# Kernel optimization log

Measured on AMD Instinct MI355X. Metric: run time of the kernel, lower is better.

## Reference

```python
import itertools
import jax, jax.numpy as jnp
import numpy as np

# static block configuration
B, C, H, W, DIM, HEADS = 2, 4, 60, 120, 512, 8
WS = (2, 6, 12)          # window size (Wc, Wh, Ww)
SS = (1, 3, 6)           # shift size
N = WS[0] * WS[1] * WS[2]            # 144 tokens per window
C1, H1, W1 = C // WS[0], H // WS[1], W // WS[2]
NW = C1 * H1 * W1                    # windows per sample
DH = DIM // HEADS
EPS = 1e-6


def _attn_bias():
    """Static shifted-window attention bias (nW, N, N): 0 within group, -inf across.
    Mirrors compute_3d_shifted_window_mask (warped=True, longitude wrap merge)."""
    img = np.zeros((C, H, W), np.int32)
    c_sl = ((0, C - WS[0]), (C - WS[0], C - SS[0]), (C - SS[0], C))
    h_sl = ((0, H - WS[1]), (H - WS[1], H - SS[1]), (H - SS[1], H))
    w_sl = ((0, W - WS[2]), (W - WS[2], W - SS[2]), (W - SS[2], W))
    cnt = 0
    for (cs, ce), (hs, he), (ws_, we) in itertools.product(c_sl, h_sl, w_sl):
        img[cs:ce, hs:he, ws_:we] = cnt
        cnt += 1
    # warped (periodic longitude) group merges
    for i in range(3):
        for a, b in ((1, 2), (4, 5), (7, 8)):
            img[img == a + 9 * i] = b + 9 * i
    m = img.reshape(C1, WS[0], H1, WS[1], W1, WS[2])
    m = m.transpose(0, 2, 4, 1, 3, 5).reshape(NW, N)
    diff = m[:, None, :] - m[:, :, None]
    return jnp.asarray(np.where(diff != 0, -np.inf, 0.0).astype(np.float32))


_BIAS = _attn_bias()[None, :, None, :, :]  # (1, nW, 1, N, N)


def _ln(x, s, b):
    mu = x.mean(-1, keepdims=True)
    var = x.var(-1, keepdims=True)
    return (x - mu) / jnp.sqrt(var + EPS) * s + b


def setup_inputs() -> dict:
    key = jax.random.key(0)
    ks = jax.random.split(key, 6)
    s = 0.02
    return {
        "x": jax.random.normal(ks[0], (B, C * H * W, DIM), jnp.float32),
        "qkv_w": jax.random.normal(ks[1], (DIM, 3 * DIM), jnp.float32) * s,
        "qkv_b": jnp.zeros((3 * DIM,), jnp.float32),
        "proj_w": jax.random.normal(ks[2], (DIM, DIM), jnp.float32) * s,
        "proj_b": jnp.zeros((DIM,), jnp.float32),
        "norm1_scale": jnp.ones((DIM,), jnp.float32),
        "norm1_bias": jnp.zeros((DIM,), jnp.float32),
        "norm2_scale": jnp.ones((DIM,), jnp.float32),
        "norm2_bias": jnp.zeros((DIM,), jnp.float32),
        "mlp_w1": jax.random.normal(ks[3], (DIM, 4 * DIM), jnp.float32) * s,
        "mlp_b1": jnp.zeros((4 * DIM,), jnp.float32),
        "mlp_w2": jax.random.normal(ks[4], (4 * DIM, DIM), jnp.float32) * s,
        "mlp_b2": jnp.zeros((DIM,), jnp.float32),
    }


def reference(x, qkv_w, qkv_b, proj_w, proj_b, norm1_scale, norm1_bias,
              norm2_scale, norm2_bias, mlp_w1, mlp_b1, mlp_w2, mlp_b2):
    shortcut = x                                   # (B, L, D)
    h = _ln(x, norm1_scale, norm1_bias).reshape(B, C, H, W, DIM)
    # cyclic shift
    h = jnp.roll(h, (-SS[0], -SS[1], -SS[2]), axis=(1, 2, 3))
    # window partition: (B,C,H,W,D) -> (B*nW, N, D)
    h = h.reshape(B, C1, WS[0], H1, WS[1], W1, WS[2], DIM)
    h = h.transpose(0, 1, 3, 5, 2, 4, 6, 7).reshape(B * NW, N, DIM)
    # windowed multi-head self-attention
    qkv = h @ qkv_w + qkv_b                        # (B*nW, N, 3*D)
    qkv = qkv.reshape(B, NW, N, 3, HEADS, DH)
    q = qkv[..., 0, :, :].transpose(0, 1, 3, 2, 4)  # (B, nW, H, N, Dh)
    k = qkv[..., 1, :, :].transpose(0, 1, 3, 2, 4)
    v = qkv[..., 2, :, :].transpose(0, 1, 3, 2, 4)
    scale = 1.0 / float(np.sqrt(DH))
    attn = jnp.einsum("bwhnd,bwhmd->bwhnm", q, k) * scale + _BIAS
    attn = jax.nn.softmax(attn, axis=-1)
    o = jnp.einsum("bwhnm,bwhmd->bwhnd", attn, v)
    o = o.transpose(0, 1, 3, 2, 4).reshape(B * NW, N, DIM)
    o = o @ proj_w + proj_b
    # window reverse: (B*nW, N, D) -> (B,C,H,W,D)
    o = o.reshape(B, C1, H1, W1, WS[0], WS[1], WS[2], DIM)
    o = o.transpose(0, 1, 4, 2, 5, 3, 6, 7).reshape(B, C, H, W, DIM)
    # reverse cyclic shift
    o = jnp.roll(o, SS, axis=(1, 2, 3))
    x = shortcut + o.reshape(B, C * H * W, DIM)    # drop_path is identity
    # MLP block
    h2 = _ln(x, norm2_scale, norm2_bias)
    h2 = jax.nn.gelu(h2 @ mlp_w1 + mlp_b1) @ mlp_w2 + mlp_b2
    return x + h2
```

## Files before the change

### kernel.cpp

```cpp
#include <hip/hip_runtime.h>

typedef __attribute__((ext_vector_type(4))) int i32x4;
typedef __attribute__((ext_vector_type(8))) short bf16x8;
typedef __attribute__((ext_vector_type(4))) float f32x4;
typedef __attribute__((ext_vector_type(8))) unsigned short u16x8;
typedef __attribute__((ext_vector_type(8))) char c8x8;

#define BAR() __builtin_amdgcn_s_barrier()
#define VMC(n) asm volatile("s_waitcnt vmcnt(" #n ")" ::: "memory")
#define SB0() __builtin_amdgcn_sched_barrier(0)
#define WAITL() do { asm volatile("s_waitcnt lgkmcnt(0)"); SB0(); } while (0)
#define DSRI(dst, base, imm) \
  asm volatile("ds_read_b128 %0, %1 offset:%2" : "=&v"(dst) : "v"(base), "i"(imm))

__device__ inline unsigned short f2bf(float f) {
  unsigned int u = __float_as_uint(f);
  u += 0x7fffu + ((u >> 16) & 1u);
  return (unsigned short)(u >> 16);
}

__device__ inline char q8(float v, float s) {
  float q = rintf(v * s);
  q = fminf(fmaxf(q, -127.0f), 127.0f);
  return (char)(int)q;
}

__device__ inline void gload_lds16(const void* g, void* l) {
  __builtin_amdgcn_global_load_lds(
      (const __attribute__((address_space(1))) void*)g,
      (__attribute__((address_space(3))) void*)l, 16, 0, 0);
}

__global__ void zero4(unsigned* p) {
  if (threadIdx.x < 4) p[threadIdx.x] = 0;
}

__global__ void wabsmax(const float* __restrict__ a, const float* __restrict__ b,
                        const float* __restrict__ c, const float* __restrict__ d,
                        unsigned* __restrict__ sc) {
  int blk = blockIdx.x;
  const float* W;
  int seg;
  size_t base;
  if (blk < 768) { W = a; seg = 0; base = (size_t)blk * 1024; }
  else if (blk < 1024) { W = b; seg = 1; base = (size_t)(blk - 768) * 1024; }
  else if (blk < 2048) { W = c; seg = 2; base = (size_t)(blk - 1024) * 1024; }
  else { W = d; seg = 3; base = (size_t)(blk - 2048) * 1024; }
  float m = 0.0f;
  #pragma unroll
  for (int i = 0; i < 4; ++i)
    m = fmaxf(m, fabsf(W[base + threadIdx.x * 4 + i]));
  #pragma unroll
  for (int o = 32; o; o >>= 1) m = fmaxf(m, __shfl_xor(m, o));
  if ((threadIdx.x & 63) == 0) atomicMax(&sc[seg], __float_as_uint(m));
}

__global__ void wtrans_all(const float* __restrict__ qkv_w,
                           const float* __restrict__ proj_w,
                           const float* __restrict__ w1,
                           const float* __restrict__ w2,
                           char* __restrict__ WqT, char* __restrict__ WpT,
                           char* __restrict__ W1T, char* __restrict__ W2T,
                           const unsigned* __restrict__ sc) {
  int idx = blockIdx.x * 256 + threadIdx.x;
  const float* W;
  char* Wt;
  int K, N, seg;
  if (idx < 786432) {
    W = qkv_w; Wt = WqT; K = 512; N = 1536; seg = 0;
  } else if (idx < 1048576) {
    idx -= 786432; W = proj_w; Wt = WpT; K = 512; N = 512; seg = 1;
  } else if (idx < 2097152) {
    idx -= 1048576; W = w1; Wt = W1T; K = 512; N = 2048; seg = 2;
  } else {
    idx -= 2097152; W = w2; Wt = W2T; K = 2048; N = 512; seg = 3;
  }
  float wabs = __uint_as_float(sc[seg]);
  int k = idx / N, n = idx - k * N;
  Wt[(size_t)n * K + k] = q8(W[idx], 127.0f / wabs);
}

template <int MODE>
__global__ void ln_k(const float* __restrict__ x, const float* __restrict__ sc,
                     const float* __restrict__ bi, char* __restrict__ o) {
  int t = blockIdx.x * 4 + (threadIdx.x >> 6);
  int l = threadIdx.x & 63;
  size_t src;
  if (MODE == 0) {
    int b = t / 28800, r = t - b * 28800;
    int win = r / 144, tok = r - win * 144;
    int c1 = win / 100, rem = win - c1 * 100;
    int h1 = rem / 10, w1 = rem - h1 * 10;
    int tc = tok / 72, tr = tok - tc * 72;
    int th = tr / 12, tw = tr - th * 12;
    int cs = c1 * 2 + tc, hs = h1 * 6 + th, wsp = w1 * 12 + tw;
    int co = (cs + 1) & 3;
    int ho = hs + 3; if (ho >= 60) ho -= 60;
    int wo = wsp + 6; if (wo >= 120) wo -= 120;
    src = ((size_t)b * 28800 + (co * 60 + ho) * 120 + wo) * 512;
  } else {
    src = (size_t)t * 512;
  }
  const float4* xr = (const float4*)(x + src);
  float4 v0 = xr[l * 2], v1 = xr[l * 2 + 1];
  float s = v0.x + v0.y + v0.z + v0.w + v1.x + v1.y + v1.z + v1.w;
  float s2 = v0.x * v0.x + v0.y * v0.y + v0.z * v0.z + v0.w * v0.w +
             v1.x * v1.x + v1.y * v1.y + v1.z * v1.z + v1.w * v1.w;
  #pragma unroll
  for (int o2 = 32; o2; o2 >>= 1) {
    s += __shfl_xor(s, o2);
    s2 += __shfl_xor(s2, o2);
  }
  float mean = s * (1.0f / 512.0f);
  float var = s2 * (1.0f / 512.0f) - mean * mean;
  float inv = rsqrtf(var + 1e-6f);
  const float4* scp = (const float4*)sc;
  const float4* bip = (const float4*)bi;
  float4 sa = scp[l * 2], sb = scp[l * 2 + 1];
  float4 ba = bip[l * 2], bb = bip[l * 2 + 1];
  const float QS = 127.0f / 6.0f;
  c8x8 ov;
  ov[0] = q8((v0.x - mean) * inv * sa.x + ba.x, QS);
  ov[1] = q8((v0.y - mean) * inv * sa.y + ba.y, QS);
  ov[2] = q8((v0.z - mean) * inv * sa.z + ba.z, QS);
  ov[3] = q8((v0.w - mean) * inv * sa.w + ba.w, QS);
  ov[4] = q8((v1.x - mean) * inv * sb.x + bb.x, QS);
  ov[5] = q8((v1.y - mean) * inv * sb.y + bb.y, QS);
  ov[6] = q8((v1.z - mean) * inv * sb.z + bb.z, QS);
  ov[7] = q8((v1.w - mean) * inv * sb.w + bb.w, QS);
  *(c8x8*)&o[(size_t)t * 512 + l * 8] = ov;
}

template <int EPI>
__launch_bounds__(256, 2)
__global__ void gemmQ(const char* __restrict__ A, const char* __restrict__ Bt,
                      const float* __restrict__ bias, void* __restrict__ outp,
                      const float* __restrict__ res,
                      const unsigned* __restrict__ scu, int widx, float ascale,
                      int M, int N, int K) {
  __shared__ __attribute__((aligned(16))) char lds3[3][24576];
  const int tid = threadIdx.x;
  const int w = tid >> 6, l = tid & 63;
  const int lane15 = l & 15;
  const int ntile = N >> 8;
  const int nwg = gridDim.x;
  const int q = nwg >> 3, r = nwg & 7;
  const int xcd = blockIdx.x & 7, idx8 = blockIdx.x >> 3;
  const int wgid = (xcd < r ? xcd * (q + 1) : r * (q + 1) + (xcd - r) * q) + idx8;
  const int bm = wgid / ntile, bn = wgid - bm * ntile;
  const int KT = K >> 6;

  const int rA0 = w * 16 + (l >> 2);
  const int rA1 = (4 + w) * 16 + (l >> 2);
  const int colx0 = ((l & 3) << 4) ^ (((rA0 >> 1) & 3) << 4);
  const int offA0 = rA0 * K + colx0;
  const int offA1 = rA1 * K + colx0;
  int offB[4];
  #pragma unroll
  for (int j = 0; j < 4; ++j) {
    int rb = (j * 4 + w) * 16 + (l >> 2);
    offB[j] = rb * K + (((l & 3) << 4) ^ (((rb >> 1) & 3) << 4));
  }

  unsigned lds0 = (unsigned)(unsigned long long)
      (__attribute__((address_space(3))) void*)(void*)&lds3[0][0];
  const unsigned comA =
      (unsigned)(lane15 * 64 + (((l >> 4) << 4) ^ (((lane15 >> 1) & 3) << 4)));
  unsigned bA0 = lds0 + comA;
  unsigned bA1 = bA0 + 24576u, bA2 = bA0 + 49152u;
  const unsigned bOffB = 8192u + ((unsigned)w << 12);
  unsigned bB0 = bA0 + bOffB, bB1 = bA1 + bOffB, bB2 = bA2 + bOffB;

  char* p0 = &lds3[0][0];
  char* p1 = &lds3[1][0];
  char* p2 = &lds3[2][0];

  const char* gA = A + (size_t)bm * 128 * K;
  const char* gB = Bt + (size_t)bn * 256 * K;

  i32x4 acc[8][4] = {};
  i32x4 afL[4], afH[4], bfr[4];

  auto STAGE = [&](char* pS, const char* ga, const char* gb) {
    gload_lds16(ga + offA0, pS + w * 1024);
    gload_lds16(ga + offA1, pS + 4096 + w * 1024);
    #pragma unroll
    for (int j = 0; j < 4; ++j)
      gload_lds16(gb + offB[j], pS + 8192 + (j * 4 + w) * 1024);
  };

  STAGE(p0, gA, gB); gA += 64; gB += 64;
  STAGE(p1, gA, gB); gA += 64; gB += 64;
  VMC(6);
  BAR();

  for (int t = 0; t < KT; ++t) {
    if (t < KT - 2) {
      STAGE(p2, gA, gB);
      gA += 64; gB += 64;
    }
    DSRI(afL[0], bA0, 0);    DSRI(afL[1], bA0, 1024);
    DSRI(afL[2], bA0, 2048); DSRI(afL[3], bA0, 3072);
    DSRI(bfr[0], bB0, 0);    DSRI(bfr[1], bB0, 1024);
    DSRI(bfr[2], bB0, 2048); DSRI(bfr[3], bB0, 3072);
    WAITL();
    DSRI(afH[0], bA0, 4096); DSRI(afH[1], bA0, 5120);
    DSRI(afH[2], bA0, 6144); DSRI(afH[3], bA0, 7168);
    SB0();
    __builtin_amdgcn_s_setprio(1);
    #pragma unroll
    for (int mf = 0; mf < 4; ++mf)
      #pragma unroll
      for (int nf = 0; nf < 4; ++nf)
        acc[mf][nf] = __builtin_amdgcn_mfma_i32_16x16x64_i8(
            afL[mf], bfr[nf], acc[mf][nf], 0, 0, 0);
    __builtin_amdgcn_s_setprio(0);
    WAITL();
    __builtin_amdgcn_s_setprio(1);
    #pragma unroll
    for (int mf = 0; mf < 4; ++mf)
      #pragma unroll
      for (int nf = 0; nf < 4; ++nf)
        acc[4 + mf][nf] = __builtin_amdgcn_mfma_i32_16x16x64_i8(
            afH[mf], bfr[nf], acc[4 + mf][nf], 0, 0, 0);
    __builtin_amdgcn_s_setprio(0);
    if (t < KT - 2) { VMC(6); } else if (t == KT - 2) { VMC(0); }
    if (t < KT - 1) BAR();
    unsigned ta = bA0; bA0 = bA1; bA1 = bA2; bA2 = ta;
    unsigned tb = bB0; bB0 = bB1; bB1 = bB2; bB2 = tb;
    char* tp = p0; p0 = p1; p1 = p2; p2 = tp;
  }

  const float wabs = __uint_as_float(scu[widx]);
  const float fs = ascale * wabs * (1.0f / 127.0f);
  float* outf = (float*)outp;
  unsigned short* outh = (unsigned short*)outp;
  char* outc = (char*)outp;
  #pragma unroll
  for (int mi = 0; mi < 8; ++mi) {
    #pragma unroll
    for (int j = 0; j < 4; ++j) {
      int grow = bm * 128 + mi * 16 + ((l >> 4) << 2) + j;
      int win = 0, tok = 0;
      size_t rowbase = 0;
      if constexpr (EPI == 0) {
        win = grow / 144;
        tok = grow - win * 144;
      } else if constexpr (EPI == 1) {
        win = grow / 144;
        tok = grow - win * 144;
        int b = win / 200, wl = win - b * 200;
        int c1 = wl / 100, rem = wl - c1 * 100;
        int h1 = rem / 10, w1 = rem - h1 * 10;
        int tc = tok / 72, tr = tok - tc * 72;
        int th = tr / 12, tw = tr - th * 12;
        int cs = c1 * 2 + tc, hs = h1 * 6 + th, wsp = w1 * 12 + tw;
        int co = (cs + 1) & 3;
        int ho = hs + 3; if (ho >= 60) ho -= 60;
        int wo = wsp + 6; if (wo >= 120) wo -= 120;
        rowbase = ((size_t)b * 28800 + (co * 60 + ho) * 120 + wo) * 512;
      }
      #pragma unroll
      for (int nf = 0; nf < 4; ++nf) {
        int gcol = bn * 256 + w * 64 + nf * 16 + lane15;
        float val = (float)acc[mi][nf][j] * fs + bias[gcol];
        if constexpr (EPI == 0) {
          int which = gcol >> 9, hd = (gcol >> 6) & 7, dh = gcol & 63;
          outh[(((size_t)(win * 3 + which) * 8 + hd) * 144 + tok) * 64 + dh] = f2bf(val);
        } else if constexpr (EPI == 1) {
          size_t oi = rowbase + gcol;
          outf[oi] = res[oi] + val;
        } else if constexpr (EPI == 2) {
          float u = 0.7978845608f * (val + 0.044715f * val * val * val);
          float g = val / (1.0f + __expf(-2.0f * u));
          outc[(size_t)grow * N + gcol] = q8(g, 127.0f / 2.75f);
        } else {
          size_t oi = (size_t)grow * N + gcol;
          outf[oi] += val;
        }
      }
    }
  }
}

__launch_bounds__(576)
__global__ void attn_k(const unsigned short* __restrict__ qkv,
                       char* __restrict__ owin) {
  __shared__ __attribute__((aligned(16))) unsigned short Ks[144 * 72];
  __shared__ __attribute__((aligned(16))) unsigned short Vt[64 * 168];
  __shared__ __attribute__((aligned(16))) unsigned short Ps[144 * 168];
  __shared__ unsigned char gid[144];
  int bid = blockIdx.x;
  int win = bid >> 3, head = bid & 7;
  const unsigned short* qb = qkv + ((size_t)(win * 3 + 0) * 8 + head) * (144 * 64);
  const unsigned short* kb = qkv + ((size_t)(win * 3 + 1) * 8 + head) * (144 * 64);
  const unsigned short* vb = qkv + ((size_t)(win * 3 + 2) * 8 + head) * (144 * 64);
  int tid = threadIdx.x;
  int wv = tid >> 6, l = tid & 63;
  int lane15 = l & 15, lk = (l >> 4) << 3;
  bf16x8 aq0 = *(const bf16x8*)(qb + (wv * 16 + lane15) * 64 + lk);
  bf16x8 aq1 = *(const bf16x8*)(qb + (wv * 16 + lane15) * 64 + 32 + lk);
  {
    int row = tid >> 2, c0 = (tid & 3) << 4;
    u16x8 ka = *(const u16x8*)(kb + row * 64 + c0);
    u16x8 kc = *(const u16x8*)(kb + row * 64 + c0 + 8);
    *(u16x8*)&Ks[row * 72 + c0] = ka;
    *(u16x8*)&Ks[row * 72 + c0 + 8] = kc;
    u16x8 va = *(const u16x8*)(vb + row * 64 + c0);
    u16x8 vc = *(const u16x8*)(vb + row * 64 + c0 + 8);
    #pragma unroll
    for (int j = 0; j < 8; ++j) Vt[(c0 + j) * 168 + row] = va[j];
    #pragma unroll
    for (int j = 0; j < 8; ++j) Vt[(c0 + 8 + j) * 168 + row] = vc[j];
  }
  for (int i = tid; i < 64 * 24; i += 576) {
    int d = i / 24, m = i - d * 24;
    Vt[d * 168 + 144 + m] = 0;
  }
  for (int i = tid; i < 144 * 24; i += 576) {
    int r = i / 24, c = i - r * 24;
    Ps[r * 168 + 144 + c] = 0;
  }
  if (tid < 144) {
    int wl = win % 200;
    int c1 = wl / 100, rem = wl - c1 * 100;
    int h1 = rem / 10, w1 = rem - h1 * 10;
    int tc = tid / 72, tr = tid - tc * 72;
    int th = tr / 12, tw = tr - th * 12;
    int cs = c1 * 2 + tc, hs = h1 * 6 + th, wsp = w1 * 12 + tw;
    int rc = cs < 2 ? 0 : (cs < 3 ? 1 : 2);
    int rh = hs < 54 ? 0 : (hs < 57 ? 1 : 2);
    int rw = wsp < 108 ? 0 : (wsp < 114 ? 1 : 2);
    if (rw == 1) rw = 2;
    gid[tid] = (unsigned char)(rc * 9 + rh * 3 + rw);
  }
  __syncthreads();
  f32x4 sf[9];
  #pragma unroll
  for (int ct = 0; ct < 9; ++ct) {
    f32x4 z = {};
    bf16x8 b0 = *(const bf16x8*)&Ks[(ct * 16 + lane15) * 72 + lk];
    bf16x8 b1 = *(const bf16x8*)&Ks[(ct * 16 + lane15) * 72 + 32 + lk];
    z = __builtin_amdgcn_mfma_f32_16x16x32_bf16(aq0, b0, z, 0, 0, 0);
    z = __builtin_amdgcn_mfma_f32_16x16x32_bf16(aq1, b1, z, 0, 0, 0);
    sf[ct] = z;
  }
  int gi[4];
  #pragma unroll
  for (int j = 0; j < 4; ++j) gi[j] = gid[wv * 16 + ((l >> 4) << 2) + j];
  float mx[4] = {-1e30f, -1e30f, -1e30f, -1e30f};
  #pragma unroll
  for (int ct = 0; ct < 9; ++ct) {
    int gj = gid[ct * 16 + lane15];
    #pragma unroll
    for (int j = 0; j < 4; ++j) {
      float s = sf[ct][j] * 0.125f;
      if (gj != gi[j]) s = -1e30f;
      sf[ct][j] = s;
      mx[j] = fmaxf(mx[j], s);
    }
  }
  #pragma unroll
  for (int o2 = 8; o2; o2 >>= 1)
    #pragma unroll
    for (int j = 0; j < 4; ++j) mx[j] = fmaxf(mx[j], __shfl_xor(mx[j], o2));
  float sm[4] = {0.f, 0.f, 0.f, 0.f};
  #pragma unroll
  for (int ct = 0; ct < 9; ++ct)
    #pragma unroll
    for (int j = 0; j < 4; ++j) {
      float e = __expf(sf[ct][j] - mx[j]);
      sf[ct][j] = e;
      sm[j] += e;
    }
  #pragma unroll
  for (int o2 = 8; o2; o2 >>= 1)
    #pragma unroll
    for (int j = 0; j < 4; ++j) sm[j] += __shfl_xor(sm[j], o2);
  float rs[4];
  #pragma unroll
  for (int j = 0; j < 4; ++j) rs[j] = 1.0f / sm[j];
  #pragma unroll
  for (int ct = 0; ct < 9; ++ct)
    #pragma unroll
    for (int j = 0; j < 4; ++j)
      Ps[(wv * 16 + ((l >> 4) << 2) + j) * 168 + ct * 16 + lane15] =
          f2bf(sf[ct][j] * rs[j]);
  __syncthreads();
  f32x4 of[4] = {};
  #pragma unroll
  for (int ks = 0; ks < 5; ++ks) {
    bf16x8 ap = *(const bf16x8*)&Ps[(wv * 16 + lane15) * 168 + ks * 32 + lk];
    #pragma unroll
    for (int nt = 0; nt < 4; ++nt) {
      bf16x8 bv = *(const bf16x8*)&Vt[(nt * 16 + lane15) * 168 + ks * 32 + lk];
      of[nt] = __builtin_amdgcn_mfma_f32_16x16x32_bf16(ap, bv, of[nt], 0, 0, 0);
    }
  }
  char* ob = owin + (size_t)win * 144 * 512 + head * 64;
  const float OS = 127.0f / 4.0f;
  #pragma unroll
  for (int nt = 0; nt < 4; ++nt)
    #pragma unroll
    for (int j = 0; j < 4; ++j) {
      int row = wv * 16 + ((l >> 4) << 2) + j;
      ob[(size_t)row * 512 + nt * 16 + lane15] = q8(of[nt][j], OS);
    }
}

extern "C" void kernel_launch(void* const* d_in, const int* in_sizes, int n_in,
                              void* d_out, int out_size, void* d_ws, size_t ws_size,
                              hipStream_t stream) {
  const float* x = (const float*)d_in[0];
  const float* qkv_w = (const float*)d_in[1];
  const float* qkv_b = (const float*)d_in[2];
  const float* proj_w = (const float*)d_in[3];
  const float* proj_b = (const float*)d_in[4];
  const float* n1s = (const float*)d_in[5];
  const float* n1b = (const float*)d_in[6];
  const float* n2s = (const float*)d_in[7];
  const float* n2b = (const float*)d_in[8];
  const float* w1 = (const float*)d_in[9];
  const float* b1 = (const float*)d_in[10];
  const float* w2 = (const float*)d_in[11];
  const float* b2 = (const float*)d_in[12];
  float* out = (float*)d_out;
  char* ws = (char*)d_ws;

  char* WqT = ws;
  char* WpT = ws + 1572864;
  char* W1T = ws + 2097152;
  char* W2T = ws + 4194304;
  unsigned* scu = (unsigned*)(ws + 5242880);
  char* hwin = ws + 6291456;
  unsigned short* qkvb = (unsigned short*)(ws + 65273856);
  char* owin = ws + 242221056;
  char* mid = ws + 65273856;

  zero4<<<1, 64, 0, stream>>>(scu);
  wabsmax<<<3072, 256, 0, stream>>>(qkv_w, proj_w, w1, w2, scu);
  wtrans_all<<<12288, 256, 0, stream>>>(qkv_w, proj_w, w1, w2,
                                        WqT, WpT, W1T, W2T, scu);
  ln_k<0><<<14400, 256, 0, stream>>>(x, n1s, n1b, hwin);
  gemmQ<0><<<450 * 6, 256, 0, stream>>>(hwin, WqT, qkv_b, qkvb, nullptr,
                                        scu, 0, 6.0f / 127.0f, 57600, 1536, 512);
  attn_k<<<3200, 576, 0, stream>>>(qkvb, owin);
  gemmQ<1><<<450 * 2, 256, 0, stream>>>(owin, WpT, proj_b, out, x,
                                        scu, 1, 4.0f / 127.0f, 57600, 512, 512);
  ln_k<1><<<14400, 256, 0, stream>>>(out, n2s, n2b, hwin);
  gemmQ<2><<<450 * 8, 256, 0, stream>>>(hwin, W1T, b1, mid, nullptr,
                                        scu, 2, 6.0f / 127.0f, 57600, 2048, 512);
  gemmQ<3><<<450 * 2, 256, 0, stream>>>(mid, W2T, b2, out, nullptr,
                                        scu, 3, 2.75f / 127.0f, 57600, 512, 2048);
}
```

Measured before the change: 768.8 us.

## Quantize V and softmax probabilities to int8 for the PV matmul

The QKV GEMM epilogue now writes the V slice as int8 with a fixed scale, and the attention kernel computes P·V with i8 MFMA (16x16x64) instead of bf16. This halves the V and P shared-memory footprint and the V global traffic, and cuts the number of K-steps. The q8 helper also switches to integer rounding and clamping. The cost is reduced accuracy: the fixed clipping at ±4 for V and the 1/127 resolution for probabilities may exceed tolerance.

```diff
diff --git a/kernel.cpp b/kernel.cpp
--- a/kernel.cpp
+++ b/kernel.cpp
@@ -20,9 +20,9 @@
 }
 
 __device__ inline char q8(float v, float s) {
-  float q = rintf(v * s);
-  q = fminf(fmaxf(q, -127.0f), 127.0f);
-  return (char)(int)q;
+  int q = __float2int_rn(v * s);
+  q = q < -127 ? -127 : (q > 127 ? 127 : q);
+  return (char)q;
 }
 
 __device__ inline void gload_lds16(const void* g, void* l) {
@@ -266,7 +266,14 @@
         float val = (float)acc[mi][nf][j] * fs + bias[gcol];
         if constexpr (EPI == 0) {
           int which = gcol >> 9, hd = (gcol >> 6) & 7, dh = gcol & 63;
-          outh[(((size_t)(win * 3 + which) * 8 + hd) * 144 + tok) * 64 + dh] = f2bf(val);
+          if (which == 2) {
+            size_t bo = ((size_t)((win * 3 + 2) * 8 + hd)) * 18432 +
+                        (size_t)tok * 64 + dh;
+            outc[bo] = q8(val, 127.0f / 4.0f);
+          } else {
+            outh[(((size_t)(win * 3 + which) * 8 + hd) * 144 + tok) * 64 + dh] =
+                f2bf(val);
+          }
         } else if constexpr (EPI == 1) {
           size_t oi = rowbase + gcol;
           outf[oi] = res[oi] + val;
@@ -287,14 +294,15 @@
 __global__ void attn_k(const unsigned short* __restrict__ qkv,
                        char* __restrict__ owin) {
   __shared__ __attribute__((aligned(16))) unsigned short Ks[144 * 72];
-  __shared__ __attribute__((aligned(16))) unsigned short Vt[64 * 168];
-  __shared__ __attribute__((aligned(16))) unsigned short Ps[144 * 168];
+  __shared__ __attribute__((aligned(16))) char Vt[64 * 208];
+  __shared__ __attribute__((aligned(16))) char Ps[144 * 208];
   __shared__ unsigned char gid[144];
   int bid = blockIdx.x;
   int win = bid >> 3, head = bid & 7;
   const unsigned short* qb = qkv + ((size_t)(win * 3 + 0) * 8 + head) * (144 * 64);
   const unsigned short* kb = qkv + ((size_t)(win * 3 + 1) * 8 + head) * (144 * 64);
-  const unsigned short* vb = qkv + ((size_t)(win * 3 + 2) * 8 + head) * (144 * 64);
+  const char* vqc = (const char*)qkv +
+                    ((size_t)((win * 3 + 2) * 8 + head)) * 18432;
   int tid = threadIdx.x;
   int wv = tid >> 6, l = tid & 63;
   int lane15 = l & 15, lk = (l >> 4) << 3;
@@ -306,20 +314,18 @@
     u16x8 kc = *(const u16x8*)(kb + row * 64 + c0 + 8);
     *(u16x8*)&Ks[row * 72 + c0] = ka;
     *(u16x8*)&Ks[row * 72 + c0 + 8] = kc;
-    u16x8 va = *(const u16x8*)(vb + row * 64 + c0);
-    u16x8 vc = *(const u16x8*)(vb + row * 64 + c0 + 8);
-    #pragma unroll
-    for (int j = 0; j < 8; ++j) Vt[(c0 + j) * 168 + row] = va[j];
-    #pragma unroll
-    for (int j = 0; j < 8; ++j) Vt[(c0 + 8 + j) * 168 + row] = vc[j];
-  }
-  for (int i = tid; i < 64 * 24; i += 576) {
-    int d = i / 24, m = i - d * 24;
-    Vt[d * 168 + 144 + m] = 0;
-  }
-  for (int i = tid; i < 144 * 24; i += 576) {
-    int r = i / 24, c = i - r * 24;
-    Ps[r * 168 + 144 + c] = 0;
+    i32x4 vv = *(const i32x4*)(vqc + row * 64 + c0);
+    const char* v8 = (const char*)&vv;
+    #pragma unroll
+    for (int j = 0; j < 16; ++j) Vt[(c0 + j) * 208 + row] = v8[j];
+  }
+  for (int i = tid; i < 64 * 48; i += 576) {
+    int d = i / 48;
+    Vt[d * 208 + 144 + (i - d * 48)] = 0;
+  }
+  for (int i = tid; i < 144 * 48; i += 576) {
+    int rr = i / 48;
+    Ps[rr * 208 + 144 + (i - rr * 48)] = 0;
   }
   if (tid < 144) {
     int wl = win % 200;
@@ -383,28 +389,32 @@
   #pragma unroll
   for (int ct = 0; ct < 9; ++ct)
     #pragma unroll
-    for (int j = 0; j < 4; ++j)
-      Ps[(wv * 16 + ((l >> 4) << 2) + j) * 168 + ct * 16 + lane15] =
-          f2bf(sf[ct][j] * rs[j]);
+    for (int j = 0; j < 4; ++j) {
+      int qrow = wv * 16 + ((l >> 4) << 2) + j;
+      Ps[qrow * 208 + ct * 16 + lane15] = q8(sf[ct][j] * rs[j], 127.0f);
+    }
   __syncthreads();
-  f32x4 of[4] = {};
-  #pragma unroll
-  for (int ks = 0; ks < 5; ++ks) {
-    bf16x8 ap = *(const bf16x8*)&Ps[(wv * 16 + lane15) * 168 + ks * 32 + lk];
+  i32x4 of4[4] = {};
+  const int qrow0 = wv * 16 + lane15;
+  const int koff = (l >> 4) << 4;
+  #pragma unroll
+  for (int ks = 0; ks < 3; ++ks) {
+    i32x4 ap = *(const i32x4*)&Ps[qrow0 * 208 + ks * 64 + koff];
     #pragma unroll
     for (int nt = 0; nt < 4; ++nt) {
-      bf16x8 bv = *(const bf16x8*)&Vt[(nt * 16 + lane15) * 168 + ks * 32 + lk];
-      of[nt] = __builtin_amdgcn_mfma_f32_16x16x32_bf16(ap, bv, of[nt], 0, 0, 0);
+      i32x4 bv = *(const i32x4*)&Vt[(nt * 16 + lane15) * 208 + ks * 64 + koff];
+      of4[nt] = __builtin_amdgcn_mfma_i32_16x16x64_i8(ap, bv, of4[nt], 0, 0, 0);
     }
   }
   char* ob = owin + (size_t)win * 144 * 512 + head * 64;
+  const float fpv = 4.0f / (127.0f * 127.0f);
   const float OS = 127.0f / 4.0f;
   #pragma unroll
   for (int nt = 0; nt < 4; ++nt)
     #pragma unroll
     for (int j = 0; j < 4; ++j) {
       int row = wv * 16 + ((l >> 4) << 2) + j;
-      ob[(size_t)row * 512 + nt * 16 + lane15] = q8(of[nt][j], OS);
+      ob[(size_t)row * 512 + nt * 16 + lane15] = q8((float)of4[nt][j] * fpv, OS);
     }
 }
 
```

Result: slower. 855.4 us (+11.3%).
